# Kernel optimization log

Measured on AMD Instinct MI355X. Metric: run time of the kernel, lower is better.

The kernel has to match this reference:

```python
import jax, jax.numpy as jnp
import numpy as np

B, C, H, W = 32, 256, 32, 32
C8 = C // 8


def setup_inputs() -> dict:
    key = jax.random.key(0)
    ks = jax.random.split(key, 8)
    s = 1.0 / np.sqrt(C)
    return {
        "x": jax.random.normal(ks[0], (B, C, H, W), dtype=jnp.float32),
        "Wq": jax.random.normal(ks[1], (C8, C), dtype=jnp.float32) * s,
        "bq": jax.random.normal(ks[2], (C8,), dtype=jnp.float32) * s,
        "Wk": jax.random.normal(ks[3], (C8, C), dtype=jnp.float32) * s,
        "bk": jax.random.normal(ks[4], (C8,), dtype=jnp.float32) * s,
        "Wv": jax.random.normal(ks[5], (C, C), dtype=jnp.float32) * s,
        "bv": jax.random.normal(ks[6], (C,), dtype=jnp.float32) * s,
        "gamma": jax.random.normal(ks[7], (1,), dtype=jnp.float32) * 0.1,
    }


def reference(x, Wq, bq, Wk, bk, Wv, bv, gamma):
    b, c, h, w = x.shape
    n = h * w
    xf = x.reshape(b, c, n)  # [B, C, N]
    # 1x1 convs == per-pixel linear projections
    q = jnp.einsum('dc,bcn->bnd', Wq, xf) + bq            # [B, N, C/8]
    k = jnp.einsum('dc,bcn->bdn', Wk, xf) + bk[:, None]    # [B, C/8, N]
    v = jnp.einsum('dc,bcn->bdn', Wv, xf) + bv[:, None]    # [B, C, N]
    energy = jnp.einsum('bnd,bdm->bnm', q, k)              # [B, N, N], no scaling (as in source)
    attn = jax.nn.softmax(energy, axis=-1)                 # softmax over keys
    # out[:, :, i] = sum_j V[:, :, j] * attn[i, j]
    out = jnp.einsum('bdn,bmn->bdm', v, attn)              # [B, C, N]
    out = out.reshape(b, c, h, w)
    return gamma * out + x
```

## Files before the change

### kernel.cpp

```cpp
#include <hip/hip_runtime.h>
#include <math.h>

#define BB 32
#define CC 256
#define CQ 32
#define NN 1024

typedef short bf16x8 __attribute__((ext_vector_type(8)));
typedef float f32x4  __attribute__((ext_vector_type(4)));
typedef unsigned short u16;

__device__ __forceinline__ u16 f2bf(float f) {
    unsigned u = __float_as_uint(f);
    u = (u + 0x7FFFu + ((u >> 16) & 1u)) >> 16;
    return (u16)u;
}

__device__ __forceinline__ unsigned cvt_pk_bf16(float lo, float hi) {
    unsigned r;
    asm("v_cvt_pk_bf16_f32 %0, %1, %2" : "=v"(r) : "v"(lo), "v"(hi));
    return r;
}

__global__ void wpack_kernel(const float* __restrict__ Wq,
                             const float* __restrict__ Wk,
                             const float* __restrict__ Wv,
                             u16* __restrict__ wfrag)
{
    const int o = blockIdx.x * 256 + threadIdx.x;
    const int j    = o & 7;
    const int lane = (o >> 3) & 63;
    const int kc   = (o >> 9) & 7;
    const int rt   = o >> 12;
    const int row  = rt * 16 + (lane & 15);
    const int col  = kc * 32 + (lane >> 4) * 8 + j;
    const float v = (row < 32) ? Wq[row * 256 + col]
                  : (row < 64) ? Wk[(row - 32) * 256 + col]
                               : Wv[(row - 64) * 256 + col];
    wfrag[o] = f2bf(v);
}

struct QSmem {
    union {
        u16 xs[32][268];
        u16 osv[CC][40];
    };
    u16 osqk[32][72];
};

__global__ __launch_bounds__(256, 4) void qkv_kernel(
    const float* __restrict__ x, const u16* __restrict__ wfrag,
    const float* __restrict__ bq, const float* __restrict__ bk,
    const float* __restrict__ bv,
    u16* __restrict__ qt, u16* __restrict__ kt, u16* __restrict__ vv)
{
    __shared__ QSmem sm;
    const int b = blockIdx.y, n0 = blockIdx.x * 32;
    const int t = threadIdx.x;
    const int lane = t & 63, w = t >> 6;
    const int quad = lane >> 4, c16 = lane & 15;

    {
        const float* xb = x + (size_t)b * CC * NN + n0;
        const int n4 = (t & 7) * 4;
        const int cr = t >> 3;
        float4 f[8];
#pragma unroll
        for (int it = 0; it < 8; ++it)
            f[it] = *(const float4*)(xb + (size_t)(it * 32 + cr) * NN + n4);
#pragma unroll
        for (int it = 0; it < 8; ++it) {
            const int c = it * 32 + cr;
            sm.xs[n4 + 0][c] = f2bf(f[it].x);
            sm.xs[n4 + 1][c] = f2bf(f[it].y);
            sm.xs[n4 + 2][c] = f2bf(f[it].z);
            sm.xs[n4 + 3][c] = f2bf(f[it].w);
        }
    }
    __syncthreads();

    f32x4 acc[5][2];
#pragma unroll
    for (int i = 0; i < 5; ++i)
#pragma unroll
        for (int j = 0; j < 2; ++j) acc[i][j] = (f32x4){0.f, 0.f, 0.f, 0.f};

#pragma unroll 2
    for (int k = 0; k < 8; ++k) {
        const int c0 = k * 32;
        bf16x8 wa[5], xb[2];
#pragma unroll
        for (int rs = 0; rs < 5; ++rs)
            wa[rs] = *(const bf16x8*)&wfrag[(size_t)(((w * 5 + rs) * 8 + k) * 64 + lane) * 8];
#pragma unroll
        for (int ns = 0; ns < 2; ++ns) {
            const short4 a = *(const short4*)&sm.xs[ns * 16 + c16][c0 + quad * 8];
            const short4 b2 = *(const short4*)&sm.xs[ns * 16 + c16][c0 + quad * 8 + 4];
            bf16x8 v;
            v[0] = a.x; v[1] = a.y; v[2] = a.z; v[3] = a.w;
            v[4] = b2.x; v[5] = b2.y; v[6] = b2.z; v[7] = b2.w;
            xb[ns] = v;
        }
#pragma unroll
        for (int rs = 0; rs < 5; ++rs)
#pragma unroll
            for (int ns = 0; ns < 2; ++ns)
                acc[rs][ns] = __builtin_amdgcn_mfma_f32_16x16x32_bf16(
                    wa[rs], xb[ns], acc[rs][ns], 0, 0, 0);
    }

    __syncthreads();

#pragma unroll
    for (int rs = 0; rs < 5; ++rs) {
#pragma unroll
        for (int r = 0; r < 4; ++r) {
            const int rg = w * 80 + rs * 16 + quad * 4 + r;
            const float bias = (rg < 32) ? bq[rg] : (rg < 64) ? bk[rg - 32] : bv[rg - 64];
#pragma unroll
            for (int ns = 0; ns < 2; ++ns) {
                const int n = ns * 16 + c16;
                const u16 h = f2bf(acc[rs][ns][r] + bias);
                if (rg < 64) sm.osqk[n][rg] = h;
                else         sm.osv[rg - 64][n] = h;
            }
        }
    }
    __syncthreads();

    {
        const int o = (t & 127) * 8;
        const int n = o >> 5, d = o & 31;
        if (t < 128) {
            const bf16x8 v = *(const bf16x8*)&sm.osqk[n][d];
            *(bf16x8*)&qt[((size_t)b * NN + n0) * CQ + n * 32 + d] = v;
        } else {
            const int p = ((n & 0x18) >> 1) | ((n & 4) << 2) | (n & 3);
            const bf16x8 v = *(const bf16x8*)&sm.osqk[n][d + 32];
            *(bf16x8*)&kt[((size_t)b * NN + n0) * CQ + p * 32 + d] = v;
        }
    }
#pragma unroll
    for (int it = 0; it < 4; ++it) {
        const int o = it * 2048 + t * 8;
        const int c = o >> 5, n = o & 31;
        const bf16x8 v = *(const bf16x8*)&sm.osv[c][n];
        *(bf16x8*)&vv[((size_t)b * CC + c) * NN + n0 + n] = v;
    }
}

__global__ __launch_bounds__(256, 2) void attn_kernel(
    const u16* __restrict__ qt, const u16* __restrict__ kt,
    const u16* __restrict__ vv, const float* __restrict__ x,
    const float* __restrict__ gamma_p, float* __restrict__ out)
{
    const int bid  = blockIdx.x;
    const int xcd  = bid & 7;
    const int slot = bid >> 3;
    const int b    = (xcd << 2) | (slot >> 4);
    const int m0b  = (slot & 15) * 64;

    const int t = threadIdx.x, lane = t & 63, w = t >> 6;
    const int quad = lane >> 4, c16 = lane & 15;
    const int m0 = m0b + (w & 1) * 32;
    const int c0 = (w >> 1) * 128;

    bf16x8 qa[2];
#pragma unroll
    for (int mt = 0; mt < 2; ++mt)
        qa[mt] = *(const bf16x8*)&qt[((size_t)b * NN + m0 + mt * 16 + c16) * CQ + quad * 8];

    bf16x8 ones;
#pragma unroll
    for (int j = 0; j < 8; ++j) ones[j] = (short)0x3F80;

    f32x4 accO[8][2];
    f32x4 lsum[2];
#pragma unroll
    for (int mt = 0; mt < 2; ++mt) {
        lsum[mt] = (f32x4){0.f, 0.f, 0.f, 0.f};
#pragma unroll
        for (int cs = 0; cs < 8; ++cs) accO[cs][mt] = (f32x4){0.f, 0.f, 0.f, 0.f};
    }

    const u16* vb = vv + (size_t)b * CC * NN;
    const u16* kp = kt + (size_t)b * NN * CQ;

    bf16x8 kbA[2], kbB[2];
#pragma unroll
    for (int tt = 0; tt < 2; ++tt)
        kbA[tt] = *(const bf16x8*)&kp[(size_t)(tt * 16 + c16) * CQ + quad * 8];

    auto CHUNK = [&](int cb, bf16x8 (&kbC)[2], bf16x8 (&kbN)[2]) {
        const int nb = cb * 32;
        bf16x8 va[8];
#pragma unroll
        for (int cs = 0; cs < 8; ++cs)
            va[cs] = *(const bf16x8*)&vb[(size_t)(c0 + cs * 16 + c16) * NN + nb + quad * 8];
        if (cb + 1 < 32) {
#pragma unroll
            for (int tt = 0; tt < 2; ++tt)
                kbN[tt] = *(const bf16x8*)&kp[(size_t)(nb + 32 + tt * 16 + c16) * CQ + quad * 8];
        }
#pragma unroll
        for (int mt = 0; mt < 2; ++mt) {
            f32x4 s0 = __builtin_amdgcn_mfma_f32_16x16x32_bf16(
                kbC[0], qa[mt], (f32x4){0.f, 0.f, 0.f, 0.f}, 0, 0, 0);
            f32x4 s1 = __builtin_amdgcn_mfma_f32_16x16x32_bf16(
                kbC[1], qa[mt], (f32x4){0.f, 0.f, 0.f, 0.f}, 0, 0, 0);
            union { unsigned u[4]; bf16x8 v; } pu;
            pu.u[0] = cvt_pk_bf16(__expf(s0[0]), __expf(s0[1]));
            pu.u[1] = cvt_pk_bf16(__expf(s0[2]), __expf(s0[3]));
            pu.u[2] = cvt_pk_bf16(__expf(s1[0]), __expf(s1[1]));
            pu.u[3] = cvt_pk_bf16(__expf(s1[2]), __expf(s1[3]));
            const bf16x8 pb = pu.v;
            lsum[mt] = __builtin_amdgcn_mfma_f32_16x16x32_bf16(ones, pb, lsum[mt], 0, 0, 0);
#pragma unroll
            for (int cs = 0; cs < 8; ++cs)
                accO[cs][mt] = __builtin_amdgcn_mfma_f32_16x16x32_bf16(
                    va[cs], pb, accO[cs][mt], 0, 0, 0);
        }
    };

#pragma unroll 1
    for (int cb = 0; cb < 32; cb += 2) {
        CHUNK(cb,     kbA, kbB);
        CHUNK(cb + 1, kbB, kbA);
    }

    const float gamma = gamma_p[0];
#pragma unroll
    for (int mt = 0; mt < 2; ++mt) {
        const float inv = gamma / lsum[mt][0];
        const int m = m0 + mt * 16 + c16;
#pragma unroll
        for (int cs = 0; cs < 8; ++cs) {
            const int cb2 = c0 + cs * 16 + quad * 4;
#pragma unroll
            for (int r = 0; r < 4; ++r) {
                const size_t idx = ((size_t)b * CC + cb2 + r) * NN + m;
                out[idx] = accO[cs][mt][r] * inv + x[idx];
            }
        }
    }
}

extern "C" void kernel_launch(void* const* d_in, const int* in_sizes, int n_in,
                              void* d_out, int out_size, void* d_ws, size_t ws_size,
                              hipStream_t stream)
{
    const float* x  = (const float*)d_in[0];
    const float* Wq = (const float*)d_in[1];
    const float* bq = (const float*)d_in[2];
    const float* Wk = (const float*)d_in[3];
    const float* bk = (const float*)d_in[4];
    const float* Wv = (const float*)d_in[5];
    const float* bv = (const float*)d_in[6];
    const float* gm = (const float*)d_in[7];
    float* out = (float*)d_out;

    u16* qt    = (u16*)d_ws;
    u16* kt    = qt + (size_t)BB * NN * CQ;
    u16* vv    = kt + (size_t)BB * NN * CQ;
    u16* wfrag = vv + (size_t)BB * CC * NN;

    wpack_kernel<<<320, 256, 0, stream>>>(Wq, Wk, Wv, wfrag);
    dim3 grid(32, BB);
    qkv_kernel<<<grid, 256, 0, stream>>>(x, wfrag, bq, bk, bv, qt, kt, vv);
    attn_kernel<<<512, 256, 0, stream>>>(qt, kt, vv, x, gm, out);
}
```

Measured before the change: 180.2 us.

## Split attention key range across waves and merge partial sums in LDS

Each block now handles 32 queries instead of 64. Its four waves split the work two ways: by channel half and by key half, and each wave covers 512 keys. The partial output accumulators and row sums are exchanged through shared memory so that each wave finishes half of its channel tiles, and the grid doubles to 1024 blocks. V loads are split into two groups of four to cut register use, and launch bounds are raised to 4 blocks per SM. The aim is higher occupancy and more parallelism in exchange for LDS traffic, a barrier, and loss of the K double-buffering.

```diff
diff --git a/kernel.cpp b/kernel.cpp
--- a/kernel.cpp
+++ b/kernel.cpp
@@ -149,21 +149,25 @@
     }
 }
 
-__global__ __launch_bounds__(256, 2) void attn_kernel(
+__global__ __launch_bounds__(256, 4) void attn_kernel(
     const u16* __restrict__ qt, const u16* __restrict__ kt,
     const u16* __restrict__ vv, const float* __restrict__ x,
     const float* __restrict__ gamma_p, float* __restrict__ out)
 {
+    __shared__ f32x4 mg[4][8][64];
+    __shared__ float lu[4][2][16];
+
     const int bid  = blockIdx.x;
     const int xcd  = bid & 7;
     const int slot = bid >> 3;
-    const int b    = (xcd << 2) | (slot >> 4);
-    const int m0b  = (slot & 15) * 64;
+    const int b    = (xcd << 2) | (slot >> 5);
+    const int m0   = (slot & 31) * 32;
 
     const int t = threadIdx.x, lane = t & 63, w = t >> 6;
     const int quad = lane >> 4, c16 = lane & 15;
-    const int m0 = m0b + (w & 1) * 32;
-    const int c0 = (w >> 1) * 128;
+    const int ch = w & 1;
+    const int nh = w >> 1;
+    const int c0 = ch * 128;
 
     bf16x8 qa[2];
 #pragma unroll
@@ -186,61 +190,88 @@
     const u16* vb = vv + (size_t)b * CC * NN;
     const u16* kp = kt + (size_t)b * NN * CQ;
 
-    bf16x8 kbA[2], kbB[2];
+    bf16x8 kb[2];
 #pragma unroll
     for (int tt = 0; tt < 2; ++tt)
-        kbA[tt] = *(const bf16x8*)&kp[(size_t)(tt * 16 + c16) * CQ + quad * 8];
-
-    auto CHUNK = [&](int cb, bf16x8 (&kbC)[2], bf16x8 (&kbN)[2]) {
-        const int nb = cb * 32;
-        bf16x8 va[8];
-#pragma unroll
-        for (int cs = 0; cs < 8; ++cs)
+        kb[tt] = *(const bf16x8*)&kp[(size_t)(nh * 512 + tt * 16 + c16) * CQ + quad * 8];
+
+#pragma unroll 1
+    for (int i = 0; i < 16; ++i) {
+        const int nb = (nh * 16 + i) * 32;
+
+        bf16x8 va[4];
+#pragma unroll
+        for (int cs = 0; cs < 4; ++cs)
             va[cs] = *(const bf16x8*)&vb[(size_t)(c0 + cs * 16 + c16) * NN + nb + quad * 8];
-        if (cb + 1 < 32) {
-#pragma unroll
-            for (int tt = 0; tt < 2; ++tt)
-                kbN[tt] = *(const bf16x8*)&kp[(size_t)(nb + 32 + tt * 16 + c16) * CQ + quad * 8];
-        }
+
+        bf16x8 pb[2];
 #pragma unroll
         for (int mt = 0; mt < 2; ++mt) {
             f32x4 s0 = __builtin_amdgcn_mfma_f32_16x16x32_bf16(
-                kbC[0], qa[mt], (f32x4){0.f, 0.f, 0.f, 0.f}, 0, 0, 0);
+                kb[0], qa[mt], (f32x4){0.f, 0.f, 0.f, 0.f}, 0, 0, 0);
             f32x4 s1 = __builtin_amdgcn_mfma_f32_16x16x32_bf16(
-                kbC[1], qa[mt], (f32x4){0.f, 0.f, 0.f, 0.f}, 0, 0, 0);
+                kb[1], qa[mt], (f32x4){0.f, 0.f, 0.f, 0.f}, 0, 0, 0);
+            if (mt == 1) {
+#pragma unroll
+                for (int tt = 0; tt < 2; ++tt)
+                    kb[tt] = *(const bf16x8*)&kp[(size_t)(nb + 32 + tt * 16 + c16) * CQ + quad * 8];
+            }
             union { unsigned u[4]; bf16x8 v; } pu;
             pu.u[0] = cvt_pk_bf16(__expf(s0[0]), __expf(s0[1]));
             pu.u[1] = cvt_pk_bf16(__expf(s0[2]), __expf(s0[3]));
             pu.u[2] = cvt_pk_bf16(__expf(s1[0]), __expf(s1[1]));
             pu.u[3] = cvt_pk_bf16(__expf(s1[2]), __expf(s1[3]));
-            const bf16x8 pb = pu.v;
-            lsum[mt] = __builtin_amdgcn_mfma_f32_16x16x32_bf16(ones, pb, lsum[mt], 0, 0, 0);
-#pragma unroll
-            for (int cs = 0; cs < 8; ++cs)
+            pb[mt] = pu.v;
+        }
+
+#pragma unroll
+        for (int mt = 0; mt < 2; ++mt)
+            lsum[mt] = __builtin_amdgcn_mfma_f32_16x16x32_bf16(ones, pb[mt], lsum[mt], 0, 0, 0);
+
+#pragma unroll
+        for (int cs = 0; cs < 4; ++cs)
+#pragma unroll
+            for (int mt = 0; mt < 2; ++mt)
                 accO[cs][mt] = __builtin_amdgcn_mfma_f32_16x16x32_bf16(
-                    va[cs], pb, accO[cs][mt], 0, 0, 0);
-        }
-    };
-
-#pragma unroll 1
-    for (int cb = 0; cb < 32; cb += 2) {
-        CHUNK(cb,     kbA, kbB);
-        CHUNK(cb + 1, kbB, kbA);
-    }
-
+                    va[cs], pb[mt], accO[cs][mt], 0, 0, 0);
+
+#pragma unroll
+        for (int cs = 0; cs < 4; ++cs)
+            va[cs] = *(const bf16x8*)&vb[(size_t)(c0 + (cs + 4) * 16 + c16) * NN + nb + quad * 8];
+
+#pragma unroll
+        for (int cs = 0; cs < 4; ++cs)
+#pragma unroll
+            for (int mt = 0; mt < 2; ++mt)
+                accO[cs + 4][mt] = __builtin_amdgcn_mfma_f32_16x16x32_bf16(
+                    va[cs], pb[mt], accO[cs + 4][mt], 0, 0, 0);
+    }
+
+    const int wk0 = nh ? 0 : 4;
+#pragma unroll
+    for (int k = 0; k < 8; ++k)
+        mg[w][k][lane] = accO[wk0 + (k >> 1)][k & 1];
+    if (quad == 0) { lu[w][0][c16] = lsum[0][0]; lu[w][1][c16] = lsum[1][0]; }
+    __syncthreads();
+
+    const int p = w ^ 2;
+    const int e0 = nh ? 4 : 0;
     const float gamma = gamma_p[0];
-#pragma unroll
-    for (int mt = 0; mt < 2; ++mt) {
-        const float inv = gamma / lsum[mt][0];
+    float inv[2];
+#pragma unroll
+    for (int mt = 0; mt < 2; ++mt)
+        inv[mt] = gamma / (lsum[mt][0] + lu[p][mt][c16]);
+
+#pragma unroll
+    for (int k = 0; k < 8; ++k) {
+        const int cs = e0 + (k >> 1), mt = k & 1;
+        const f32x4 o = accO[cs][mt] + mg[p][k][lane];
         const int m = m0 + mt * 16 + c16;
-#pragma unroll
-        for (int cs = 0; cs < 8; ++cs) {
-            const int cb2 = c0 + cs * 16 + quad * 4;
-#pragma unroll
-            for (int r = 0; r < 4; ++r) {
-                const size_t idx = ((size_t)b * CC + cb2 + r) * NN + m;
-                out[idx] = accO[cs][mt][r] * inv + x[idx];
-            }
+        const int cb2 = c0 + cs * 16 + quad * 4;
+#pragma unroll
+        for (int r = 0; r < 4; ++r) {
+            const size_t idx = ((size_t)b * CC + cb2 + r) * NN + m;
+            out[idx] = o[r] * inv[mt] + x[idx];
         }
     }
 }
@@ -267,5 +298,5 @@
     wpack_kernel<<<320, 256, 0, stream>>>(Wq, Wk, Wv, wfrag);
     dim3 grid(32, BB);
     qkv_kernel<<<grid, 256, 0, stream>>>(x, wfrag, bq, bk, bv, qt, kt, vv);
-    attn_kernel<<<512, 256, 0, stream>>>(qt, kt, vv, x, gm, out);
-}
+    attn_kernel<<<1024, 256, 0, stream>>>(qt, kt, vv, x, gm, out);
+}
```

After: 198.4 us. +10.1%, slower.
